# Optimization experiments

Measured on AMD Instinct MI355X. Metric: run time of the kernel, lower is better.

The kernel has to match this reference:

```python
import jax, jax.numpy as jnp
import numpy as np

NX, NTEST, DX, DY = 8192, 8192, 32, 32
VAR_EPS = 0.01   # params['var_eps']
L_MEAN = 8.0     # fit kernel lengthscale after l_scale adjustment
L_VAR = 8.0


def _rbf(X, Y, l):
    # pairwise squared distances: [Nx, Nq]
    d2 = (jnp.sum(X * X, axis=1)[:, None]
          + jnp.sum(Y * Y, axis=1)[None, :]
          - 2.0 * (X @ Y.T))
    return jnp.exp(-jnp.maximum(d2, 0.0) / (2.0 * l * l))


def setup_inputs() -> dict:
    key = jax.random.key(0)
    ks = jax.random.split(key, 10)
    inp = {
        'x_mu':   jax.random.normal(ks[0], (NTEST, DX), jnp.float32),
        'y_eta':  jax.random.normal(ks[1], (NTEST, DY), jnp.float32),
        'y_mean': jax.random.normal(ks[2], (NTEST, DY), jnp.float32),
        'y_var':  jax.random.normal(ks[3], (NTEST, DY), jnp.float32) * 0.1,
        'X_mean': jax.random.normal(ks[4], (NX, DX + DY), jnp.float32),
        'X_var':  jax.random.normal(ks[5], (NX, DX + 2 * DY), jnp.float32),
        'Z_mean': jax.random.normal(ks[6], (NX, DY), jnp.float32),
        'Z_var':  jax.random.normal(ks[7], (NX, DY), jnp.float32),
        # precomputed inverse Gram matrices (stand-ins with same compute pattern)
        'kXXmean_inv': jax.random.normal(ks[8], (NX, NX), jnp.float32) * 0.001,
        'kXXvar_inv':  jax.random.normal(ks[9], (NX, NX), jnp.float32) * 0.001,
    }
    return inp


def reference(x_mu, y_eta, y_mean, y_var, X_mean, X_var, Z_mean, Z_var,
              kXXmean_inv, kXXvar_inv):
    # map_mean: x_mean = [x_mu, y_mean + y_var]
    x_mean = jnp.concatenate([x_mu, y_mean + y_var], axis=1)          # [Nq, DX+DY]
    Lambda_mean = kXXmean_inv @ Z_mean                                # [Nx, DY]
    z_mean = _rbf(X_mean, x_mean, L_MEAN).T @ Lambda_mean             # [Nq, DY]

    # map_var: x_var = [x_mu, var_eps * flip(y_eta), y_mean + y_var]
    x_var = jnp.concatenate(
        [x_mu, VAR_EPS * jnp.flip(y_eta, axis=0), y_mean + y_var], axis=1)
    Lambda_var = kXXvar_inv @ Z_var                                   # [Nx, DY]
    z_var = _rbf(X_var, x_var, L_VAR).T @ Lambda_var                  # [Nq, DY]

    # transported sample: (y_mean + z_mean) + (y_var + z_var)
    return (y_mean + z_mean) + (y_var + z_var)
```

## Files before the change

kernel.cpp:

```cpp
#include <hip/hip_runtime.h>
#include <stdint.h>

#define NXR 8192
#define NQR 8192
#define DMEAN 64
#define DVAR 96
#define DYC 32

typedef float f32x4 __attribute__((ext_vector_type(4)));
typedef __bf16 bf16x8 __attribute__((ext_vector_type(8)));
typedef unsigned short us4v __attribute__((ext_vector_type(4)));

__device__ __forceinline__ unsigned short f2bf(float f) {
    union { float f; uint32_t u; } v; v.f = f;
    uint32_t r = (v.u + 0x7FFFu + ((v.u >> 16) & 1u)) >> 16;
    return (unsigned short)r;
}
__device__ __forceinline__ float bf2f(unsigned short b) {
    union { uint32_t u; float f; } v; v.u = ((uint32_t)b) << 16;
    return v.f;
}
__device__ __forceinline__ int perm_idx(int k, int c) {
    return (k >> 5) * 1024 + (c >> 4) * 512 +
           ((((k >> 3) & 3) * 16 + (c & 15)) * 8) + (k & 7);
}

__global__ __launch_bounds__(256) void k_prep(
    const float* __restrict__ x_mu, const float* __restrict__ y_eta,
    const float* __restrict__ y_mean, const float* __restrict__ y_var,
    const float* __restrict__ X_mean, const float* __restrict__ X_var,
    const float* __restrict__ Z_mean, const float* __restrict__ Z_var,
    unsigned short* __restrict__ Qm, unsigned short* __restrict__ Qv,
    unsigned short* __restrict__ Xm, unsigned short* __restrict__ Xv,
    unsigned short* __restrict__ Zpm, unsigned short* __restrict__ Zpv,
    float* __restrict__ qn_m, float* __restrict__ qn_v,
    float* __restrict__ Xn_m, float* __restrict__ Xn_v,
    float* __restrict__ lam_f32, float* __restrict__ out)
{
    int tid = blockIdx.x * 256 + threadIdx.x;
    lam_f32[tid] = 0.0f;
    int w = threadIdx.x >> 6;
    int lane = threadIdx.x & 63;
    int row = blockIdx.x * 4 + w;

    float accq_m = 0.f, accq_v = 0.f;
    if (lane < 32) {
        int c = lane;
        float xm = x_mu[row * 32 + c];
        float s  = y_mean[row * 32 + c] + y_var[row * 32 + c];
        float e  = 0.01f * y_eta[(NQR - 1 - row) * 32 + c];
        unsigned short bx = f2bf(xm), bs = f2bf(s), be = f2bf(e);
        Qm[row * DMEAN + c] = bx;  Qm[row * DMEAN + 32 + c] = bs;
        Qv[row * DVAR + c] = bx;   Qv[row * DVAR + 32 + c] = be;
        Qv[row * DVAR + 64 + c] = bs;
        out[row * 32 + c] = s;
        Zpm[perm_idx(row, c)] = f2bf(Z_mean[row * 32 + c]);
        Zpv[perm_idx(row, c)] = f2bf(Z_var[row * 32 + c]);
        float fx = bf2f(bx), fs = bf2f(bs), fe = bf2f(be);
        accq_m = fx * fx + fs * fs;
        accq_v = fx * fx + fe * fe + fs * fs;
    }
    float a = X_mean[row * DMEAN + lane];
    unsigned short ba = f2bf(a);
    Xm[row * DMEAN + lane] = ba;
    float fa = bf2f(ba);
    float accx_m = fa * fa;

    float b0 = X_var[row * DVAR + lane];
    unsigned short bb0 = f2bf(b0);
    Xv[row * DVAR + lane] = bb0;
    float fb0 = bf2f(bb0);
    float accx_v = fb0 * fb0;
    if (lane < 32) {
        float b1 = X_var[row * DVAR + 64 + lane];
        unsigned short bb1 = f2bf(b1);
        Xv[row * DVAR + 64 + lane] = bb1;
        float fb1 = bf2f(bb1);
        accx_v += fb1 * fb1;
    }
    for (int o = 32; o >= 1; o >>= 1) {
        accq_m += __shfl_xor(accq_m, o, 64);
        accq_v += __shfl_xor(accq_v, o, 64);
        accx_m += __shfl_xor(accx_m, o, 64);
        accx_v += __shfl_xor(accx_v, o, 64);
    }
    if (lane == 0) {
        qn_m[row] = accq_m; qn_v[row] = accq_v;
        Xn_m[row] = accx_m; Xn_v[row] = accx_v;
    }
}

__global__ __launch_bounds__(256) void k_lambda(
    const float* __restrict__ kXXm, const float* __restrict__ kXXv,
    const unsigned short* __restrict__ Zpm, const unsigned short* __restrict__ Zpv,
    float* __restrict__ lam_f32)
{
    int b = blockIdx.x;
    int mat = b & 1;
    int split = (b >> 1) & 1;
    int rb = b >> 2;
    const float* A = mat ? kXXv : kXXm;
    const unsigned short* Zp = mat ? Zpv : Zpm;
    float* lam = lam_f32 + mat * (NXR * DYC);

    int w = threadIdx.x >> 6, lane = threadIdx.x & 63;
    int r0 = rb * 64 + w * 16;
    int arow = r0 + (lane & 15);
    int kgrp = (lane >> 4) * 8;
    const float* Arow = A + (size_t)arow * NXR;

    f32x4 acc0 = {0.f, 0.f, 0.f, 0.f}, acc1 = {0.f, 0.f, 0.f, 0.f};
#pragma unroll 2
    for (int kb = 0; kb < 128; ++kb) {
        int kbase = split * 4096 + kb * 32;
        int k = kbase + kgrp;
        const f32x4* p = (const f32x4*)(Arow + k);
        f32x4 a0 = p[0], a1 = p[1];
        union { unsigned short u[8]; bf16x8 v; } af;
#pragma unroll
        for (int j = 0; j < 4; ++j) { af.u[j] = f2bf(a0[j]); af.u[4 + j] = f2bf(a1[j]); }
        const unsigned short* zb = Zp + (size_t)(kbase >> 5) * 1024 + lane * 8;
        bf16x8 bz0 = *(const bf16x8*)(zb);
        bf16x8 bz1 = *(const bf16x8*)(zb + 512);
        acc0 = __builtin_amdgcn_mfma_f32_16x16x32_bf16(af.v, bz0, acc0, 0, 0, 0);
        acc1 = __builtin_amdgcn_mfma_f32_16x16x32_bf16(af.v, bz1, acc1, 0, 0, 0);
    }
    int rbase = r0 + (lane >> 4) * 4;
    int c0 = lane & 15;
#pragma unroll
    for (int r = 0; r < 4; ++r) {
        atomicAdd(&lam[(rbase + r) * DYC + c0], acc0[r]);
        atomicAdd(&lam[(rbase + r) * DYC + c0 + 16], acc1[r]);
    }
}

__global__ __launch_bounds__(256) void k_pack(
    const float* __restrict__ lam_f32,
    unsigned short* __restrict__ Lpm, unsigned short* __restrict__ Lpv)
{
    int t = blockIdx.x * 256 + threadIdx.x;
    int mat = t >> 18;
    int rem = t & 262143;
    int x = rem >> 5, c = rem & 31;
    unsigned short v = f2bf(lam_f32[t]);
    (mat ? Lpv : Lpm)[perm_idx(x, c)] = v;
}

__global__ __launch_bounds__(256) void k_transport(
    const unsigned short* __restrict__ Qm, const unsigned short* __restrict__ Qv,
    const unsigned short* __restrict__ Xm, const unsigned short* __restrict__ Xv,
    const float* __restrict__ qn_m, const float* __restrict__ qn_v,
    const float* __restrict__ Xn_m, const float* __restrict__ Xn_v,
    const unsigned short* __restrict__ Lpm, const unsigned short* __restrict__ Lpv,
    float* __restrict__ out)
{
    __shared__ unsigned short KT[4][16 * 40];
    int b = blockIdx.x;
    int mat = b & 1;
    int split = (b >> 1) & 3;
    int qb = b >> 3;
    const unsigned short* Q = mat ? Qv : Qm;
    const unsigned short* X = mat ? Xv : Xm;
    const float* qn = mat ? qn_v : qn_m;
    const float* Xn = mat ? Xn_v : Xn_m;
    const unsigned short* Lp = mat ? Lpv : Lpm;
    const int D = mat ? DVAR : DMEAN;
    const int nk0 = mat ? 3 : 2;

    int w = threadIdx.x >> 6, lane = threadIdx.x & 63;
    int q0 = qb * 64 + w * 16;
    int qrow = q0 + (lane & 15);
    int g = lane >> 4;

    bf16x8 Qf[3];
    for (int c0 = 0; c0 < nk0; ++c0)
        Qf[c0] = *(const bf16x8*)(Q + (size_t)qrow * D + c0 * 32 + g * 8);
    float qn_c = qn[qrow];
    unsigned short* lds = KT[w];

    f32x4 z0 = {0.f, 0.f, 0.f, 0.f}, z1 = {0.f, 0.f, 0.f, 0.f};
    for (int xb = 0; xb < 64; ++xb) {
        int x0 = split * 2048 + xb * 32;
#pragma unroll
        for (int sub = 0; sub < 2; ++sub) {
            int xrow = x0 + sub * 16 + (lane & 15);
            const unsigned short* Xr = X + (size_t)xrow * D + g * 8;
            f32x4 s = {0.f, 0.f, 0.f, 0.f};
            s = __builtin_amdgcn_mfma_f32_16x16x32_bf16(*(const bf16x8*)(Xr), Qf[0], s, 0, 0, 0);
            s = __builtin_amdgcn_mfma_f32_16x16x32_bf16(*(const bf16x8*)(Xr + 32), Qf[1], s, 0, 0, 0);
            if (nk0 == 3)
                s = __builtin_amdgcn_mfma_f32_16x16x32_bf16(*(const bf16x8*)(Xr + 64), Qf[2], s, 0, 0, 0);
            int xnb = x0 + sub * 16 + g * 4;
            f32x4 xn4 = *(const f32x4*)(Xn + xnb);
            us4v kv;
#pragma unroll
            for (int r = 0; r < 4; ++r) {
                float d2 = xn4[r] + qn_c - 2.0f * s[r];
                d2 = fmaxf(d2, 0.0f);
                kv[r] = f2bf(__expf(-d2 * 0.0078125f));
            }
            *(us4v*)(lds + (lane & 15) * 40 + sub * 16 + g * 4) = kv;
        }
        asm volatile("s_waitcnt lgkmcnt(0)" ::: "memory");
        bf16x8 Kf = *(const bf16x8*)(lds + (lane & 15) * 40 + g * 8);
        const unsigned short* lpb = Lp + (size_t)(x0 >> 5) * 1024 + lane * 8;
        bf16x8 l0 = *(const bf16x8*)(lpb);
        bf16x8 l1 = *(const bf16x8*)(lpb + 512);
        z0 = __builtin_amdgcn_mfma_f32_16x16x32_bf16(Kf, l0, z0, 0, 0, 0);
        z1 = __builtin_amdgcn_mfma_f32_16x16x32_bf16(Kf, l1, z1, 0, 0, 0);
    }
    int rbase = q0 + g * 4;
    int c0 = lane & 15;
#pragma unroll
    for (int r = 0; r < 4; ++r) {
        atomicAdd(&out[(rbase + r) * 32 + c0], z0[r]);
        atomicAdd(&out[(rbase + r) * 32 + c0 + 16], z1[r]);
    }
}

extern "C" void kernel_launch(void* const* d_in, const int* in_sizes, int n_in,
                              void* d_out, int out_size, void* d_ws, size_t ws_size,
                              hipStream_t stream) {
    const float* x_mu   = (const float*)d_in[0];
    const float* y_eta  = (const float*)d_in[1];
    const float* y_mean = (const float*)d_in[2];
    const float* y_var  = (const float*)d_in[3];
    const float* X_mean = (const float*)d_in[4];
    const float* X_var  = (const float*)d_in[5];
    const float* Z_mean = (const float*)d_in[6];
    const float* Z_var  = (const float*)d_in[7];
    const float* kXXm   = (const float*)d_in[8];
    const float* kXXv   = (const float*)d_in[9];
    float* out = (float*)d_out;

    char* ws = (char*)d_ws;
    size_t off = 0;
    auto carve = [&](size_t bytes) { char* p = ws + off; off += (bytes + 255) & ~(size_t)255; return p; };
    unsigned short* Qm  = (unsigned short*)carve(NQR * DMEAN * 2);
    unsigned short* Qv  = (unsigned short*)carve(NQR * DVAR * 2);
    unsigned short* Xm  = (unsigned short*)carve(NXR * DMEAN * 2);
    unsigned short* Xv  = (unsigned short*)carve(NXR * DVAR * 2);
    unsigned short* Zpm = (unsigned short*)carve(NXR * DYC * 2);
    unsigned short* Zpv = (unsigned short*)carve(NXR * DYC * 2);
    unsigned short* Lpm = (unsigned short*)carve(NXR * DYC * 2);
    unsigned short* Lpv = (unsigned short*)carve(NXR * DYC * 2);
    float* qn_m = (float*)carve(NQR * 4);
    float* qn_v = (float*)carve(NQR * 4);
    float* Xn_m = (float*)carve(NXR * 4);
    float* Xn_v = (float*)carve(NXR * 4);
    float* lam_f32 = (float*)carve(2 * NXR * DYC * 4);

    k_prep<<<dim3(2048), dim3(256), 0, stream>>>(
        x_mu, y_eta, y_mean, y_var, X_mean, X_var, Z_mean, Z_var,
        Qm, Qv, Xm, Xv, Zpm, Zpv, qn_m, qn_v, Xn_m, Xn_v, lam_f32, out);
    k_lambda<<<dim3(512), dim3(256), 0, stream>>>(kXXm, kXXv, Zpm, Zpv, lam_f32);
    k_pack<<<dim3(2048), dim3(256), 0, stream>>>(lam_f32, Lpm, Lpv);
    k_transport<<<dim3(1024), dim3(256), 0, stream>>>(
        Qm, Qv, Xm, Xv, qn_m, qn_v, Xn_m, Xn_v, Lpm, Lpv, out);
}
```

Baseline: 712.5 us.

## Double the K-splits and software-prefetch loads in lambda and transport kernels

The lambda GEMM now splits K four ways instead of two and handles 64 K values per iteration. Its loop holds register double-buffering that prefetches the next A rows and Z fragments while the current ones are converted and multiplied. The transport kernel splits the X dimension eight ways instead of four and hoists the Lambda and Xn loads to the top of each iteration so they overlap the distance MFMAs. Both kernels get occupancy hints through launch bounds. The aim is more concurrent blocks on the 256 CUs and better latency hiding for the memory-bound kXX read, at the cost of more atomic adds to the outputs and higher register pressure.

```diff
diff --git a/kernel.cpp b/kernel.cpp
--- a/kernel.cpp
+++ b/kernel.cpp
@@ -90,15 +90,15 @@
     }
 }
 
-__global__ __launch_bounds__(256) void k_lambda(
+__global__ __launch_bounds__(256, 4) void k_lambda(
     const float* __restrict__ kXXm, const float* __restrict__ kXXv,
     const unsigned short* __restrict__ Zpm, const unsigned short* __restrict__ Zpv,
     float* __restrict__ lam_f32)
 {
     int b = blockIdx.x;
     int mat = b & 1;
-    int split = (b >> 1) & 1;
-    int rb = b >> 2;
+    int split = (b >> 1) & 3;
+    int rb = b >> 3;
     const float* A = mat ? kXXv : kXXm;
     const unsigned short* Zp = mat ? Zpv : Zpm;
     float* lam = lam_f32 + mat * (NXR * DYC);
@@ -106,26 +106,50 @@
     int w = threadIdx.x >> 6, lane = threadIdx.x & 63;
     int r0 = rb * 64 + w * 16;
     int arow = r0 + (lane & 15);
-    int kgrp = (lane >> 4) * 8;
-    const float* Arow = A + (size_t)arow * NXR;
+    int g = lane >> 4;
+    const float* Arow = A + (size_t)arow * NXR + (size_t)split * 2048 + g * 8;
+    const unsigned short* Zbase = Zp + (size_t)(split * 2048 >> 5) * 1024 + lane * 8;
 
     f32x4 acc0 = {0.f, 0.f, 0.f, 0.f}, acc1 = {0.f, 0.f, 0.f, 0.f};
+
+    f32x4 ca0 = *(const f32x4*)(Arow);
+    f32x4 ca1 = *(const f32x4*)(Arow + 4);
+    f32x4 ca2 = *(const f32x4*)(Arow + 32);
+    f32x4 ca3 = *(const f32x4*)(Arow + 36);
+    bf16x8 cz0 = *(const bf16x8*)(Zbase);
+    bf16x8 cz1 = *(const bf16x8*)(Zbase + 512);
+    bf16x8 cz2 = *(const bf16x8*)(Zbase + 1024);
+    bf16x8 cz3 = *(const bf16x8*)(Zbase + 1536);
+
 #pragma unroll 2
-    for (int kb = 0; kb < 128; ++kb) {
-        int kbase = split * 4096 + kb * 32;
-        int k = kbase + kgrp;
-        const f32x4* p = (const f32x4*)(Arow + k);
-        f32x4 a0 = p[0], a1 = p[1];
-        union { unsigned short u[8]; bf16x8 v; } af;
-#pragma unroll
-        for (int j = 0; j < 4; ++j) { af.u[j] = f2bf(a0[j]); af.u[4 + j] = f2bf(a1[j]); }
-        const unsigned short* zb = Zp + (size_t)(kbase >> 5) * 1024 + lane * 8;
-        bf16x8 bz0 = *(const bf16x8*)(zb);
-        bf16x8 bz1 = *(const bf16x8*)(zb + 512);
-        acc0 = __builtin_amdgcn_mfma_f32_16x16x32_bf16(af.v, bz0, acc0, 0, 0, 0);
-        acc1 = __builtin_amdgcn_mfma_f32_16x16x32_bf16(af.v, bz1, acc1, 0, 0, 0);
-    }
-    int rbase = r0 + (lane >> 4) * 4;
+    for (int kb = 0; kb < 32; ++kb) {
+        int nkb = (kb < 31) ? (kb + 1) : 31;
+        const float* An = Arow + nkb * 64;
+        const unsigned short* Zn = Zbase + (size_t)nkb * 2048;
+        f32x4 na0 = *(const f32x4*)(An);
+        f32x4 na1 = *(const f32x4*)(An + 4);
+        f32x4 na2 = *(const f32x4*)(An + 32);
+        f32x4 na3 = *(const f32x4*)(An + 36);
+        bf16x8 nz0 = *(const bf16x8*)(Zn);
+        bf16x8 nz1 = *(const bf16x8*)(Zn + 512);
+        bf16x8 nz2 = *(const bf16x8*)(Zn + 1024);
+        bf16x8 nz3 = *(const bf16x8*)(Zn + 1536);
+
+        union { unsigned short u[8]; bf16x8 v; } f0, f1;
+#pragma unroll
+        for (int j = 0; j < 4; ++j) {
+            f0.u[j] = f2bf(ca0[j]); f0.u[4 + j] = f2bf(ca1[j]);
+            f1.u[j] = f2bf(ca2[j]); f1.u[4 + j] = f2bf(ca3[j]);
+        }
+        acc0 = __builtin_amdgcn_mfma_f32_16x16x32_bf16(f0.v, cz0, acc0, 0, 0, 0);
+        acc1 = __builtin_amdgcn_mfma_f32_16x16x32_bf16(f0.v, cz1, acc1, 0, 0, 0);
+        acc0 = __builtin_amdgcn_mfma_f32_16x16x32_bf16(f1.v, cz2, acc0, 0, 0, 0);
+        acc1 = __builtin_amdgcn_mfma_f32_16x16x32_bf16(f1.v, cz3, acc1, 0, 0, 0);
+
+        ca0 = na0; ca1 = na1; ca2 = na2; ca3 = na3;
+        cz0 = nz0; cz1 = nz1; cz2 = nz2; cz3 = nz3;
+    }
+    int rbase = r0 + g * 4;
     int c0 = lane & 15;
 #pragma unroll
     for (int r = 0; r < 4; ++r) {
@@ -146,7 +170,7 @@
     (mat ? Lpv : Lpm)[perm_idx(x, c)] = v;
 }
 
-__global__ __launch_bounds__(256) void k_transport(
+__global__ __launch_bounds__(256, 8) void k_transport(
     const unsigned short* __restrict__ Qm, const unsigned short* __restrict__ Qv,
     const unsigned short* __restrict__ Xm, const unsigned short* __restrict__ Xv,
     const float* __restrict__ qn_m, const float* __restrict__ qn_v,
@@ -157,8 +181,8 @@
     __shared__ unsigned short KT[4][16 * 40];
     int b = blockIdx.x;
     int mat = b & 1;
-    int split = (b >> 1) & 3;
-    int qb = b >> 3;
+    int split = (b >> 1) & 7;
+    int qb = b >> 4;
     const unsigned short* Q = mat ? Qv : Qm;
     const unsigned short* X = mat ? Xv : Xm;
     const float* qn = mat ? qn_v : qn_m;
@@ -179,8 +203,13 @@
     unsigned short* lds = KT[w];
 
     f32x4 z0 = {0.f, 0.f, 0.f, 0.f}, z1 = {0.f, 0.f, 0.f, 0.f};
-    for (int xb = 0; xb < 64; ++xb) {
-        int x0 = split * 2048 + xb * 32;
+    for (int xb = 0; xb < 32; ++xb) {
+        int x0 = split * 1024 + xb * 32;
+        const unsigned short* lpb = Lp + (size_t)(x0 >> 5) * 1024 + lane * 8;
+        bf16x8 l0 = *(const bf16x8*)(lpb);
+        bf16x8 l1 = *(const bf16x8*)(lpb + 512);
+        f32x4 xn4a = *(const f32x4*)(Xn + x0 + g * 4);
+        f32x4 xn4b = *(const f32x4*)(Xn + x0 + 16 + g * 4);
 #pragma unroll
         for (int sub = 0; sub < 2; ++sub) {
             int xrow = x0 + sub * 16 + (lane & 15);
@@ -190,8 +219,7 @@
             s = __builtin_amdgcn_mfma_f32_16x16x32_bf16(*(const bf16x8*)(Xr + 32), Qf[1], s, 0, 0, 0);
             if (nk0 == 3)
                 s = __builtin_amdgcn_mfma_f32_16x16x32_bf16(*(const bf16x8*)(Xr + 64), Qf[2], s, 0, 0, 0);
-            int xnb = x0 + sub * 16 + g * 4;
-            f32x4 xn4 = *(const f32x4*)(Xn + xnb);
+            f32x4 xn4 = sub ? xn4b : xn4a;
             us4v kv;
 #pragma unroll
             for (int r = 0; r < 4; ++r) {
@@ -203,9 +231,6 @@
         }
         asm volatile("s_waitcnt lgkmcnt(0)" ::: "memory");
         bf16x8 Kf = *(const bf16x8*)(lds + (lane & 15) * 40 + g * 8);
-        const unsigned short* lpb = Lp + (size_t)(x0 >> 5) * 1024 + lane * 8;
-        bf16x8 l0 = *(const bf16x8*)(lpb);
-        bf16x8 l1 = *(const bf16x8*)(lpb + 512);
         z0 = __builtin_amdgcn_mfma_f32_16x16x32_bf16(Kf, l0, z0, 0, 0, 0);
         z1 = __builtin_amdgcn_mfma_f32_16x16x32_bf16(Kf, l1, z1, 0, 0, 0);
     }
@@ -253,8 +278,8 @@
     k_prep<<<dim3(2048), dim3(256), 0, stream>>>(
         x_mu, y_eta, y_mean, y_var, X_mean, X_var, Z_mean, Z_var,
         Qm, Qv, Xm, Xv, Zpm, Zpv, qn_m, qn_v, Xn_m, Xn_v, lam_f32, out);
-    k_lambda<<<dim3(512), dim3(256), 0, stream>>>(kXXm, kXXv, Zpm, Zpv, lam_f32);
+    k_lambda<<<dim3(1024), dim3(256), 0, stream>>>(kXXm, kXXv, Zpm, Zpv, lam_f32);
     k_pack<<<dim3(2048), dim3(256), 0, stream>>>(lam_f32, Lpm, Lpv);
-    k_transport<<<dim3(1024), dim3(256), 0, stream>>>(
+    k_transport<<<dim3(2048), dim3(256), 0, stream>>>(
         Qm, Qv, Xm, Xv, qn_m, qn_v, Xn_m, Xn_v, Lpm, Lpv, out);
 }
```

Result: no change. 714.2 us (+0.2%).
